# Optimization experiments

Hardware: AMD Instinct MI355X
Metric: run time of the kernel (lower is better)

## Reference

```python
import jax, jax.numpy as jnp
import numpy as np

B = 16384   # batched decode steps (have_action_batch across transitions)
H = 1024    # hidden_dim
A = 20      # len(ner_map) + 2 valid-action vocabulary


def setup_inputs() -> dict:
    key = jax.random.key(0)
    ks = jax.random.split(key, 10)
    scale = 0.02
    buffer_h = jax.random.normal(ks[0], (B, H), jnp.float32)
    stack_h = jax.random.normal(ks[1], (B, H), jnp.float32)
    output_h = jax.random.normal(ks[2], (B, H), jnp.float32)
    action_h = jax.random.normal(ks[3], (B, H), jnp.float32)
    W1 = jax.random.normal(ks[4], (4 * H, H), jnp.float32) * scale  # lstms_output_2_softmax
    b1 = jnp.zeros((H,), jnp.float32)
    W2 = jax.random.normal(ks[5], (H, A), jnp.float32) * scale      # output_2_act
    b2 = jnp.zeros((A,), jnp.float32)
    real_actions = jax.random.randint(ks[6], (B,), 0, A, dtype=jnp.int32)
    valid_mask = jax.random.bernoulli(ks[7], 0.5, (B, A))
    # gold action must always be in the valid-action list
    valid_mask = valid_mask.at[jnp.arange(B), real_actions].set(True)
    return {
        "buffer_h": buffer_h, "stack_h": stack_h, "output_h": output_h,
        "action_h": action_h, "W1": W1, "b1": b1, "W2": W2, "b2": b2,
        "valid_mask": valid_mask, "real_actions": real_actions,
    }


def reference(buffer_h, stack_h, output_h, action_h, W1, b1, W2, b2, valid_mask, real_actions):
    # ragged concat of per-example LSTM states -> [B, 4H]
    x = jnp.concatenate([buffer_h, stack_h, output_h, action_h], axis=1)
    hidden = jnp.tanh(x @ W1 + b1)          # lstms_output_2_softmax + tanh, [B, H]
    logits = hidden @ W2 + b2               # output_2_act, [B, A]
    # per-example valid-action gather expressed as masked log_softmax
    NEG = jnp.asarray(-1e9, logits.dtype)
    masked = jnp.where(valid_mask, logits, NEG)
    log_probs = jax.nn.log_softmax(masked, axis=-1)
    predict_actions = jnp.argmax(log_probs, axis=-1)               # [B] int
    losses = jnp.take_along_axis(log_probs, real_actions[:, None].astype(jnp.int32), axis=1)[:, 0]
    return predict_actions, losses
```

## Files before the change

### kernel.cpp

```cpp
#include <hip/hip_runtime.h>
#include <math.h>


#define BTOT 16384
#define HD   1024
#define NACT 20
#define KTOT 4096
#define KT_N 128

typedef __attribute__((ext_vector_type(8))) short short8;
typedef __attribute__((ext_vector_type(4))) float f32x4;

#define MFMA(a, b, c) __builtin_amdgcn_mfma_f32_16x16x32_bf16((a), (b), (c), 0, 0, 0)

__device__ __forceinline__ void gload16(const void* g, void* l)
{
    auto gp = (const __attribute__((address_space(1))) unsigned int*)((uintptr_t)g);
    auto lp = (__attribute__((address_space(3))) unsigned int*)((uintptr_t)l);
    __builtin_amdgcn_global_load_lds(gp, lp, 16, 0, 0);
}

__device__ __forceinline__ void split8(const float4 v0, const float4 v1,
                                       int4& hi, int4& lo)
{
    const float f[8] = {v0.x, v0.y, v0.z, v0.w, v1.x, v1.y, v1.z, v1.w};
    unsigned hp[4], lp[4];
#pragma unroll
    for (int i = 0; i < 4; ++i) {
        const unsigned u0 = __float_as_uint(f[2 * i]);
        const unsigned u1 = __float_as_uint(f[2 * i + 1]);
        const unsigned r0 = u0 + 0x7FFFu + ((u0 >> 16) & 1u);
        const unsigned r1 = u1 + 0x7FFFu + ((u1 >> 16) & 1u);
        hp[i] = (r0 >> 16) | (r1 & 0xFFFF0000u);
        const float h0 = __uint_as_float(r0 & 0xFFFF0000u);
        const float h1 = __uint_as_float(r1 & 0xFFFF0000u);
        const float d0 = f[2 * i] - h0;
        const float d1 = f[2 * i + 1] - h1;
        const unsigned s0 = __float_as_uint(d0);
        const unsigned s1 = __float_as_uint(d1);
        const unsigned q0 = s0 + 0x7FFFu + ((s0 >> 16) & 1u);
        const unsigned q1 = s1 + 0x7FFFu + ((s1 >> 16) & 1u);
        lp[i] = (q0 >> 16) | (q1 & 0xFFFF0000u);
    }
    hi = make_int4((int)hp[0], (int)hp[1], (int)hp[2], (int)hp[3]);
    lo = make_int4((int)lp[0], (int)lp[1], (int)lp[2], (int)lp[3]);
}

__global__ __launch_bounds__(256) void detect_mask_kernel(
    const unsigned int* __restrict__ w, int nwords, int* __restrict__ ctr)
{
    int c0 = 0, c1 = 0, c2 = 0, c3 = 0;
    for (int i = blockIdx.x * 256 + threadIdx.x; i < nwords; i += gridDim.x * 256) {
        unsigned int v = w[i];
        c0 += (v & 0x000000FFu) ? 1 : 0;
        c1 += (v & 0x0000FF00u) ? 1 : 0;
        c2 += (v & 0x00FF0000u) ? 1 : 0;
        c3 += (v & 0xFF000000u) ? 1 : 0;
    }
#pragma unroll
    for (int off = 32; off; off >>= 1) {
        c0 += __shfl_xor(c0, off, 64);
        c1 += __shfl_xor(c1, off, 64);
        c2 += __shfl_xor(c2, off, 64);
        c3 += __shfl_xor(c3, off, 64);
    }
    if ((threadIdx.x & 63) == 0) {
        atomicAdd(&ctr[0], c0);
        atomicAdd(&ctr[1], c1);
        atomicAdd(&ctr[2], c2);
        atomicAdd(&ctr[3], c3);
    }
}

__global__ __launch_bounds__(256) void wpack_kernel(
    const float* __restrict__ W1, char* __restrict__ Wp)
{
    const int b  = blockIdx.x;
    const int t  = threadIdx.x;
    const int nt = b >> 7;
    const int kt = b & 127;
    const int nn = t & 127;
    const int h  = t >> 7;

    float f[16];
#pragma unroll
    for (int kk = 0; kk < 16; ++kk)
        f[kk] = W1[(size_t)(kt * 32 + h * 16 + kk) * HD + nt * 128 + nn];

    int4 hi0, lo0, hi1, lo1;
    split8(make_float4(f[0], f[1], f[2], f[3]),
           make_float4(f[4], f[5], f[6], f[7]), hi0, lo0);
    split8(make_float4(f[8], f[9], f[10], f[11]),
           make_float4(f[12], f[13], f[14], f[15]), hi1, lo1);

    char* rowp = Wp + (((size_t)(nt * KT_N + kt)) << 14) + nn * 128;
    const int r7 = nn & 7;
    const int s0 = ((2 * h) ^ r7) << 4;
    const int s1 = ((2 * h + 1) ^ r7) << 4;
    *(int4*)(rowp + s0)        = hi0;
    *(int4*)(rowp + s1)        = hi1;
    *(int4*)(rowp + (s0 ^ 64)) = lo0;
    *(int4*)(rowp + (s1 ^ 64)) = lo1;
}


#define PHASE(AP)                                                                   \
    {                                                                               \
        const short8 ah0 = *(const short8*)(bufc + (aBase + (2*(AP)) * 2048));      \
        const short8 al0 = *(const short8*)(bufc + ((aBase + (2*(AP)) * 2048) ^ 64)); \
        const short8 ah1 = *(const short8*)(bufc + (aBase + (2*(AP)+1) * 2048));    \
        const short8 al1 = *(const short8*)(bufc + ((aBase + (2*(AP)+1) * 2048) ^ 64)); \
        __builtin_amdgcn_s_setprio(1);                                              \
        _Pragma("unroll")                                                           \
        for (int nf = 0; nf < 4; ++nf) {                                            \
            acc[2*(AP)][nf]   = MFMA(ah0, bh[nf], acc[2*(AP)][nf]);                 \
            acc[2*(AP)][nf]   = MFMA(ah0, bl[nf], acc[2*(AP)][nf]);                 \
            acc[2*(AP)][nf]   = MFMA(al0, bh[nf], acc[2*(AP)][nf]);                 \
            acc[2*(AP)+1][nf] = MFMA(ah1, bh[nf], acc[2*(AP)+1][nf]);               \
            acc[2*(AP)+1][nf] = MFMA(ah1, bl[nf], acc[2*(AP)+1][nf]);               \
            acc[2*(AP)+1][nf] = MFMA(al1, bh[nf], acc[2*(AP)+1][nf]);               \
        }                                                                           \
        __builtin_amdgcn_s_setprio(0);                                              \
    }

__global__ __launch_bounds__(512, 1) void gemm1_mfma_kernel(
    const float* __restrict__ A0, const float* __restrict__ A1,
    const float* __restrict__ A2, const float* __restrict__ A3,
    const char* __restrict__ Wp, const float* __restrict__ b1,
    float* __restrict__ hidden)
{
    extern __shared__ __align__(16) char smem[];

    const int newbid = (blockIdx.x & 7) * 32 + (blockIdx.x >> 3);
    const int mt = newbid >> 2;
    const int nt = newbid & 3;

    const int t    = threadIdx.x;
    const int lane = t & 63;
    const int wid  = t >> 6;
    const int wr = wid >> 2, wc = wid & 3;
    const int lrow = lane & 15;
    const int lk   = lane >> 4;

    const int stag = (wid ^ (wid >> 2)) & 1;

    const int rowL  = t >> 1;
    const int khalf = t & 1;
    const size_t aRowOff = (size_t)(mt * 256 + rowL) * HD;

    const char* gB0 = Wp + (((size_t)((nt * 2)     * KT_N)) << 14);
    const char* gB1 = Wp + (((size_t)((nt * 2 + 1) * KT_N)) << 14);

    const unsigned aBase = (unsigned)(wr * 128 + lrow) * 128
                         + (((unsigned)lk ^ (unsigned)(lrow & 7)) << 4);
    const unsigned bBase = (unsigned)(wc >> 1) * 16384
                         + (unsigned)((wc & 1) * 64 + lrow) * 128
                         + (((unsigned)lk ^ (unsigned)(lrow & 7)) << 4);

    const int r7 = rowL & 7;
    const unsigned wA0 = (unsigned)rowL * 128 + (((unsigned)(2 * khalf)     ^ (unsigned)r7) << 4);
    const unsigned wA1 = (unsigned)rowL * 128 + (((unsigned)(2 * khalf + 1) ^ (unsigned)r7) << 4);

    f32x4 acc[8][4];
#pragma unroll
    for (int i = 0; i < 8; ++i)
#pragma unroll
        for (int j = 0; j < 4; ++j) acc[i][j] = (f32x4){0.f, 0.f, 0.f, 0.f};

    {
        const float4* ap = (const float4*)(A0 + aRowOff + khalf * 16);
        const float4 f0 = ap[0], f1 = ap[1], f2 = ap[2], f3 = ap[3];
        int4 h0, l0, h1, l1;
        split8(f0, f1, h0, l0);
        split8(f2, f3, h1, l1);
        char* lA = smem;
        *(int4*)(lA + wA0)        = h0;
        *(int4*)(lA + (wA0 ^ 64)) = l0;
        *(int4*)(lA + wA1)        = h1;
        *(int4*)(lA + (wA1 ^ 64)) = l1;
        char* lB = smem + 32768;
        gload16(gB0 + t * 16,        lB + t * 16);
        gload16(gB0 + 8192 + t * 16, lB + 8192 + t * 16);
        gload16(gB1 + t * 16,        lB + 16384 + t * 16);
        gload16(gB1 + 8192 + t * 16, lB + 24576 + t * 16);
    }
    __syncthreads();

    for (int kt = 0; kt < KT_N; ++kt) {
        const int cur = kt & 1;
        const char* bufc  = smem + cur * 65536;
        const char* bufcB = bufc + 32768;
        char*       bufn  = smem + (cur ^ 1) * 65536;
        const bool pref = (kt + 1 < KT_N);

        float4 f0, f1, f2, f3;
        if (pref) {
            char* lB = bufn + 32768;
            const char* s0 = gB0 + (((size_t)(kt + 1)) << 14);
            const char* s1 = gB1 + (((size_t)(kt + 1)) << 14);
            gload16(s0 + t * 16,        lB + t * 16);
            gload16(s0 + 8192 + t * 16, lB + 8192 + t * 16);
            gload16(s1 + t * 16,        lB + 16384 + t * 16);
            gload16(s1 + 8192 + t * 16, lB + 24576 + t * 16);
            const int kg = (kt + 1) * 32 + khalf * 16;
            const float* seg = (kg < 1024) ? A0 : (kg < 2048) ? A1 : (kg < 3072) ? A2 : A3;
            const float4* ap = (const float4*)(seg + aRowOff + (kg & 1023));
            f0 = ap[0]; f1 = ap[1]; f2 = ap[2]; f3 = ap[3];
        }

        short8 bh[4], bl[4];
#pragma unroll
        for (int nf = 0; nf < 4; ++nf) {
            bh[nf] = *(const short8*)(bufcB + (bBase + nf * 2048));
            bl[nf] = *(const short8*)(bufcB + ((bBase + nf * 2048) ^ 64));
        }

        if (stag == 0) {
            PHASE(0) PHASE(1) PHASE(2) PHASE(3)
        } else {
            PHASE(2) PHASE(3) PHASE(0) PHASE(1)
        }

        if (pref) {
            int4 h0, l0, h1, l1;
            split8(f0, f1, h0, l0);
            split8(f2, f3, h1, l1);
            char* wAp = bufn;
            *(int4*)(wAp + wA0)        = h0;
            *(int4*)(wAp + (wA0 ^ 64)) = l0;
            *(int4*)(wAp + wA1)        = h1;
            *(int4*)(wAp + (wA1 ^ 64)) = l1;
        }
        __syncthreads();
    }

#pragma unroll
    for (int nf = 0; nf < 4; ++nf) {
        const int col = nt * 256 + wc * 64 + nf * 16 + lrow;
        const float bias = b1[col];
#pragma unroll
        for (int mf = 0; mf < 8; ++mf) {
            const int row0 = mt * 256 + wr * 128 + mf * 16 + lk * 4;
#pragma unroll
            for (int r = 0; r < 4; ++r)
                hidden[(size_t)(row0 + r) * HD + col] = tanhf(acc[mf][nf][r] + bias);
        }
    }
}

__device__ __forceinline__ void finish_row(
    const float* __restrict__ acc, const float* __restrict__ b2,
    const void* __restrict__ mask, const int* __restrict__ real_actions,
    int fmt, int row, float* __restrict__ out,
    int* __restrict__ flagCnt, int* __restrict__ flagList, int lane)
{
    float masked[NACT];
#pragma unroll
    for (int a = 0; a < NACT; ++a) {
        const float lg = acc[a] + b2[a];
        bool valid;
        if (fmt == 0)      valid = ((const unsigned char*)mask)[(size_t)row * NACT + a] != 0;
        else if (fmt == 1) valid = ((const int*)mask)[(size_t)row * NACT + a] != 0;
        else               valid = ((const float*)mask)[(size_t)row * NACT + a] != 0.f;
        masked[a] = valid ? lg : -1e9f;
    }
    float m = masked[0], m2 = -3e38f;
    int amax = 0;
#pragma unroll
    for (int a = 1; a < NACT; ++a) {
        const float v = masked[a];
        if (v > m) { m2 = m; m = v; amax = a; }
        else if (v > m2) m2 = v;
    }
    float s = 0.f;
#pragma unroll
    for (int a = 0; a < NACT; ++a) s += expf(masked[a] - m);
    const float lse = m + logf(s);
    const int ga = real_actions[row];
    float gl = masked[0];
#pragma unroll
    for (int a = 1; a < NACT; ++a) gl = (ga == a) ? masked[a] : gl;
    if (lane == 0) {
        out[row] = (float)amax;
        out[BTOT + row] = gl - lse;
        if (flagList != nullptr && (m - m2) < 1e-3f) {
            const int ix = atomicAdd(flagCnt, 1);
            flagList[ix] = row;
        }
    }
}

__global__ __launch_bounds__(256) void head_kernel(
    const float* __restrict__ hidden, const float* __restrict__ W2,
    const float* __restrict__ b2, const void* __restrict__ mask,
    const int* __restrict__ real_actions, int* __restrict__ ctr,
    int* __restrict__ flagList, float* __restrict__ out, int rowBase)
{
    const int lane = threadIdx.x & 63;
    const int lr0  = (blockIdx.x * 4 + (threadIdx.x >> 6)) * 2;

    float a0[NACT], a1[NACT];
#pragma unroll
    for (int a = 0; a < NACT; ++a) { a0[a] = 0.f; a1[a] = 0.f; }

    const float* h0 = hidden + (size_t)lr0 * HD;
    const float* h1 = h0 + HD;
#pragma unroll 4
    for (int j = 0; j < 16; ++j) {
        const int h = lane + 64 * j;
        const float hv0 = h0[h];
        const float hv1 = h1[h];
        const float4* w4 = (const float4*)(W2 + (size_t)h * NACT);
        const float4 w0 = w4[0], w1 = w4[1], w2 = w4[2], w3 = w4[3], w4v = w4[4];
        a0[0]  = fmaf(hv0, w0.x,  a0[0]);  a1[0]  = fmaf(hv1, w0.x,  a1[0]);
        a0[1]  = fmaf(hv0, w0.y,  a0[1]);  a1[1]  = fmaf(hv1, w0.y,  a1[1]);
        a0[2]  = fmaf(hv0, w0.z,  a0[2]);  a1[2]  = fmaf(hv1, w0.z,  a1[2]);
        a0[3]  = fmaf(hv0, w0.w,  a0[3]);  a1[3]  = fmaf(hv1, w0.w,  a1[3]);
        a0[4]  = fmaf(hv0, w1.x,  a0[4]);  a1[4]  = fmaf(hv1, w1.x,  a1[4]);
        a0[5]  = fmaf(hv0, w1.y,  a0[5]);  a1[5]  = fmaf(hv1, w1.y,  a1[5]);
        a0[6]  = fmaf(hv0, w1.z,  a0[6]);  a1[6]  = fmaf(hv1, w1.z,  a1[6]);
        a0[7]  = fmaf(hv0, w1.w,  a0[7]);  a1[7]  = fmaf(hv1, w1.w,  a1[7]);
        a0[8]  = fmaf(hv0, w2.x,  a0[8]);  a1[8]  = fmaf(hv1, w2.x,  a1[8]);
        a0[9]  = fmaf(hv0, w2.y,  a0[9]);  a1[9]  = fmaf(hv1, w2.y,  a1[9]);
        a0[10] = fmaf(hv0, w2.z,  a0[10]); a1[10] = fmaf(hv1, w2.z,  a1[10]);
        a0[11] = fmaf(hv0, w2.w,  a0[11]); a1[11] = fmaf(hv1, w2.w,  a1[11]);
        a0[12] = fmaf(hv0, w3.x,  a0[12]); a1[12] = fmaf(hv1, w3.x,  a1[12]);
        a0[13] = fmaf(hv0, w3.y,  a0[13]); a1[13] = fmaf(hv1, w3.y,  a1[13]);
        a0[14] = fmaf(hv0, w3.z,  a0[14]); a1[14] = fmaf(hv1, w3.z,  a1[14]);
        a0[15] = fmaf(hv0, w3.w,  a0[15]); a1[15] = fmaf(hv1, w3.w,  a1[15]);
        a0[16] = fmaf(hv0, w4v.x, a0[16]); a1[16] = fmaf(hv1, w4v.x, a1[16]);
        a0[17] = fmaf(hv0, w4v.y, a0[17]); a1[17] = fmaf(hv1, w4v.y, a1[17]);
        a0[18] = fmaf(hv0, w4v.z, a0[18]); a1[18] = fmaf(hv1, w4v.z, a1[18]);
        a0[19] = fmaf(hv0, w4v.w, a0[19]); a1[19] = fmaf(hv1, w4v.w, a1[19]);
    }
#pragma unroll
    for (int off = 32; off; off >>= 1) {
#pragma unroll
        for (int a = 0; a < NACT; ++a) {
            a0[a] += __shfl_xor(a0[a], off, 64);
            a1[a] += __shfl_xor(a1[a], off, 64);
        }
    }

    const int c1 = ctr[1], c2 = ctr[2], c3 = ctr[3];
    const int fmt = (c1 > 0) ? 0 : ((c2 > 0 || c3 > 0) ? 2 : 1);

    finish_row(a0, b2, mask, real_actions, fmt, rowBase + lr0,     out, &ctr[4], flagList, lane);
    finish_row(a1, b2, mask, real_actions, fmt, rowBase + lr0 + 1, out, &ctr[4], flagList, lane);
}

__global__ __launch_bounds__(256) void refine_hidden_kernel(
    const float* __restrict__ A0, const float* __restrict__ A1,
    const float* __restrict__ A2, const float* __restrict__ A3,
    const float* __restrict__ W1, const float* __restrict__ b1,
    const int* __restrict__ ctr, const int* __restrict__ list,
    float* __restrict__ hiddenR, int cap)
{
    __shared__ float xs[2][KTOT];
    __shared__ float red[2][4][64];
    const int tid = threadIdx.x;
    int count = ctr[4]; if (count > cap) count = cap;
    const int total = ((count + 1) >> 1) << 4;

    for (int u = blockIdx.x; u < total; u += gridDim.x) {
        const int p  = u >> 4;
        const int f0 = 2 * p;
        const int f1 = (2 * p + 1 < count) ? (2 * p + 1) : f0;
        const int r0 = list[f0];
        const int r1 = list[f1];
        const int colBase = (u & 15) << 6;

        for (int i = tid; i < KTOT; i += 256) {
            const float* seg = (i < 1024) ? A0 : (i < 2048) ? A1 : (i < 3072) ? A2 : A3;
            xs[0][i] = seg[(size_t)r0 * HD + (i & 1023)];
            xs[1][i] = seg[(size_t)r1 * HD + (i & 1023)];
        }
        __syncthreads();

        const int col   = colBase + (tid & 63);
        const int kbase = (tid >> 6) << 10;
        const float* Wc = W1 + col;
        float acc0 = 0.f, acc1 = 0.f;

        float wa[16], wb[16];
#pragma unroll
        for (int v = 0; v < 16; ++v) wa[v] = Wc[(size_t)(kbase + v) * HD];
#pragma unroll
        for (int v = 0; v < 16; ++v) wb[v] = Wc[(size_t)(kbase + 16 + v) * HD];

        const int kend = kbase + 1024;
        for (int k0 = kbase; k0 < kend; k0 += 32) {
#pragma unroll
            for (int v = 0; v < 16; ++v) {
                acc0 = fmaf(xs[0][k0 + v], wa[v], acc0);
                acc1 = fmaf(xs[1][k0 + v], wa[v], acc1);
            }
            if (k0 + 32 < kend) {
#pragma unroll
                for (int v = 0; v < 16; ++v)
                    wa[v] = Wc[(size_t)(k0 + 32 + v) * HD];
            }
#pragma unroll
            for (int v = 0; v < 16; ++v) {
                acc0 = fmaf(xs[0][k0 + 16 + v], wb[v], acc0);
                acc1 = fmaf(xs[1][k0 + 16 + v], wb[v], acc1);
            }
            if (k0 + 48 < kend) {
#pragma unroll
                for (int v = 0; v < 16; ++v)
                    wb[v] = Wc[(size_t)(k0 + 48 + v) * HD];
            }
        }

        red[0][tid >> 6][tid & 63] = acc0;
        red[1][tid >> 6][tid & 63] = acc1;
        __syncthreads();

        if (tid < 128) {
            const int r = tid >> 6, c = tid & 63;
            const float s = red[r][0][c] + red[r][1][c] + red[r][2][c] + red[r][3][c];
            const int f = r ? f1 : f0;
            hiddenR[(size_t)f * HD + colBase + c] = tanhf(s + b1[colBase + c]);
        }
        __syncthreads();
    }
}

__global__ __launch_bounds__(256) void refine_head_kernel(
    const float* __restrict__ hiddenR, const float* __restrict__ W2,
    const float* __restrict__ b2, const void* __restrict__ mask,
    const int* __restrict__ real_actions, const int* __restrict__ ctr,
    const int* __restrict__ list, float* __restrict__ out, int cap)
{
    const int lane = threadIdx.x & 63;
    const int wv   = threadIdx.x >> 6;
    int count = ctr[4]; if (count > cap) count = cap;
    const int c1 = ctr[1], c2 = ctr[2], c3 = ctr[3];
    const int fmt = (c1 > 0) ? 0 : ((c2 > 0 || c3 > 0) ? 2 : 1);

    for (int f = blockIdx.x * 4 + wv; f < count; f += gridDim.x * 4) {
        const int row = list[f];
        const float* hrow = hiddenR + (size_t)f * HD;
        float a20[NACT];
#pragma unroll
        for (int a = 0; a < NACT; ++a) a20[a] = 0.f;
#pragma unroll 4
        for (int m = 0; m < 16; ++m) {
            const int h = lane + 64 * m;
            const float hv = hrow[h];
            const float4* w4 = (const float4*)(W2 + (size_t)h * NACT);
            const float4 w0 = w4[0], w1 = w4[1], w2 = w4[2], w3 = w4[3], w4v = w4[4];
            a20[0]  = fmaf(hv, w0.x,  a20[0]);  a20[1]  = fmaf(hv, w0.y,  a20[1]);
            a20[2]  = fmaf(hv, w0.z,  a20[2]);  a20[3]  = fmaf(hv, w0.w,  a20[3]);
            a20[4]  = fmaf(hv, w1.x,  a20[4]);  a20[5]  = fmaf(hv, w1.y,  a20[5]);
            a20[6]  = fmaf(hv, w1.z,  a20[6]);  a20[7]  = fmaf(hv, w1.w,  a20[7]);
            a20[8]  = fmaf(hv, w2.x,  a20[8]);  a20[9]  = fmaf(hv, w2.y,  a20[9]);
            a20[10] = fmaf(hv, w2.z,  a20[10]); a20[11] = fmaf(hv, w2.w,  a20[11]);
            a20[12] = fmaf(hv, w3.x,  a20[12]); a20[13] = fmaf(hv, w3.y,  a20[13]);
            a20[14] = fmaf(hv, w3.z,  a20[14]); a20[15] = fmaf(hv, w3.w,  a20[15]);
            a20[16] = fmaf(hv, w4v.x, a20[16]); a20[17] = fmaf(hv, w4v.y, a20[17]);
            a20[18] = fmaf(hv, w4v.z, a20[18]); a20[19] = fmaf(hv, w4v.w, a20[19]);
        }
#pragma unroll
        for (int off = 32; off; off >>= 1) {
#pragma unroll
            for (int a = 0; a < NACT; ++a) a20[a] += __shfl_xor(a20[a], off, 64);
        }
        finish_row(a20, b2, mask, real_actions, fmt, row, out, nullptr, nullptr, lane);
    }
}

extern "C" void kernel_launch(void* const* d_in, const int* in_sizes, int n_in,
                              void* d_out, int out_size, void* d_ws, size_t ws_size,
                              hipStream_t stream)
{
    const float* buf_h = (const float*)d_in[0];
    const float* stk_h = (const float*)d_in[1];
    const float* out_h = (const float*)d_in[2];
    const float* act_h = (const float*)d_in[3];
    const float* W1    = (const float*)d_in[4];
    const float* b1    = (const float*)d_in[5];
    const float* W2    = (const float*)d_in[6];
    const float* b2    = (const float*)d_in[7];
    const void*  mask  = d_in[8];
    const int*   ra    = (const int*)d_in[9];
    float*       out   = (float*)d_out;

    int*  ctr      = (int*)d_ws;
    int*  flagList = (int*)((char*)d_ws + 256);
    char* Wp       = (char*)d_ws + 256 + 65536;
    const size_t wpBytes = (size_t)8 * KT_N * 16384;
    float* hidden  = (float*)(Wp + wpBytes);

    hipMemsetAsync(d_ws, 0, 256, stream);
    detect_mask_kernel<<<64, 256, 0, stream>>>(
        (const unsigned int*)mask, BTOT * NACT / 4, ctr);
    wpack_kernel<<<8 * KT_N, 256, 0, stream>>>(W1, Wp);

    hipFuncSetAttribute((const void*)gemm1_mfma_kernel,
                        hipFuncAttributeMaxDynamicSharedMemorySize, 131072);

    gemm1_mfma_kernel<<<256, 512, 131072, stream>>>(
        buf_h, stk_h, out_h, act_h, Wp, b1, hidden);
    head_kernel<<<BTOT / 8, 256, 0, stream>>>(
        hidden, W2, b2, mask, ra, ctr, flagList, out, 0);

    float* hiddenR = hidden;
    refine_hidden_kernel<<<2048, 256, 0, stream>>>(
        buf_h, stk_h, out_h, act_h, W1, b1, ctr, flagList, hiddenR, BTOT);
    refine_head_kernel<<<64, 256, 0, stream>>>(
        hiddenR, W2, b2, mask, ra, ctr, flagList, out, BTOT);
}
```

Measured before the change: 528.5 us.

## Prefetch A tile two steps ahead and remap blocks to XCDs by column tile

The GEMM1 main loop now loads the fp32 A tile two k-steps ahead into rotating registers and splits and writes it to LDS before the MFMA phase, not after. This gives global load latency a full iteration to resolve and takes the split/LDS store off the tail behind the MFMAs. The block-to-tile mapping also changes so each XCD handles a single N tile and half of the M tiles, which changes L2 sharing of W and A. The cost is extra registers for the second A buffer under a 512-thread, one-block launch bound, which may cause spills.

```diff
diff --git a/kernel.cpp b/kernel.cpp
--- a/kernel.cpp
+++ b/kernel.cpp
@@ -123,6 +123,46 @@
         __builtin_amdgcn_s_setprio(0);                                              \
     }
 
+#define STEP(KT, CUR, NXT)                                                          \
+    {                                                                               \
+        const int curb = (KT) & 1;                                                  \
+        const char* bufc  = smem + curb * 65536;                                    \
+        const char* bufcB = bufc + 32768;                                           \
+        char*       bufn  = smem + (curb ^ 1) * 65536;                              \
+        if ((KT) + 2 < KT_N) {                                                      \
+            const int kg = ((KT) + 2) * 32 + khalf * 16;                            \
+            const float* seg = (kg < 1024) ? A0 : (kg < 2048) ? A1                  \
+                               : (kg < 3072) ? A2 : A3;                             \
+            const float4* ap = (const float4*)(seg + aRowOff + (kg & 1023));        \
+            NXT[0] = ap[0]; NXT[1] = ap[1]; NXT[2] = ap[2]; NXT[3] = ap[3];         \
+        }                                                                           \
+        if ((KT) + 1 < KT_N) {                                                      \
+            char* lB = bufn + 32768;                                                \
+            const char* s0 = gB0 + (((size_t)((KT) + 1)) << 14);                    \
+            const char* s1 = gB1 + (((size_t)((KT) + 1)) << 14);                    \
+            gload16(s0 + t * 16,        lB + t * 16);                               \
+            gload16(s0 + 8192 + t * 16, lB + 8192 + t * 16);                        \
+            gload16(s1 + t * 16,        lB + 16384 + t * 16);                       \
+            gload16(s1 + 8192 + t * 16, lB + 24576 + t * 16);                       \
+            int4 h0, l0, h1, l1;                                                    \
+            split8(CUR[0], CUR[1], h0, l0);                                         \
+            split8(CUR[2], CUR[3], h1, l1);                                         \
+            *(int4*)(bufn + wA0)        = h0;                                       \
+            *(int4*)(bufn + (wA0 ^ 64)) = l0;                                       \
+            *(int4*)(bufn + wA1)        = h1;                                       \
+            *(int4*)(bufn + (wA1 ^ 64)) = l1;                                       \
+        }                                                                           \
+        short8 bh[4], bl[4];                                                        \
+        _Pragma("unroll")                                                           \
+        for (int nf = 0; nf < 4; ++nf) {                                            \
+            bh[nf] = *(const short8*)(bufcB + (bBase + nf * 2048));                 \
+            bl[nf] = *(const short8*)(bufcB + ((bBase + nf * 2048) ^ 64));          \
+        }                                                                           \
+        if (stag == 0) { PHASE(0) PHASE(1) PHASE(2) PHASE(3) }                      \
+        else           { PHASE(2) PHASE(3) PHASE(0) PHASE(1) }                      \
+        __syncthreads();                                                            \
+    }
+
 __global__ __launch_bounds__(512, 1) void gemm1_mfma_kernel(
     const float* __restrict__ A0, const float* __restrict__ A1,
     const float* __restrict__ A2, const float* __restrict__ A3,
@@ -131,9 +171,9 @@
 {
     extern __shared__ __align__(16) char smem[];
 
-    const int newbid = (blockIdx.x & 7) * 32 + (blockIdx.x >> 3);
-    const int mt = newbid >> 2;
-    const int nt = newbid & 3;
+    const int xcd = blockIdx.x & 7;
+    const int nt  = xcd & 3;
+    const int mt  = (blockIdx.x >> 3) + ((xcd >> 2) << 5);
 
     const int t    = threadIdx.x;
     const int lane = t & 63;
@@ -167,17 +207,20 @@
 #pragma unroll
         for (int j = 0; j < 4; ++j) acc[i][j] = (f32x4){0.f, 0.f, 0.f, 0.f};
 
+    float4 rA0[4], rA1[4];
+
     {
         const float4* ap = (const float4*)(A0 + aRowOff + khalf * 16);
         const float4 f0 = ap[0], f1 = ap[1], f2 = ap[2], f3 = ap[3];
         int4 h0, l0, h1, l1;
         split8(f0, f1, h0, l0);
         split8(f2, f3, h1, l1);
-        char* lA = smem;
-        *(int4*)(lA + wA0)        = h0;
-        *(int4*)(lA + (wA0 ^ 64)) = l0;
-        *(int4*)(lA + wA1)        = h1;
-        *(int4*)(lA + (wA1 ^ 64)) = l1;
+        *(int4*)(smem + wA0)        = h0;
+        *(int4*)(smem + (wA0 ^ 64)) = l0;
+        *(int4*)(smem + wA1)        = h1;
+        *(int4*)(smem + (wA1 ^ 64)) = l1;
+        const float4* ap1 = (const float4*)(A0 + aRowOff + 32 + khalf * 16);
+        rA0[0] = ap1[0]; rA0[1] = ap1[1]; rA0[2] = ap1[2]; rA0[3] = ap1[3];
         char* lB = smem + 32768;
         gload16(gB0 + t * 16,        lB + t * 16);
         gload16(gB0 + 8192 + t * 16, lB + 8192 + t * 16);
@@ -186,52 +229,9 @@
     }
     __syncthreads();
 
-    for (int kt = 0; kt < KT_N; ++kt) {
-        const int cur = kt & 1;
-        const char* bufc  = smem + cur * 65536;
-        const char* bufcB = bufc + 32768;
-        char*       bufn  = smem + (cur ^ 1) * 65536;
-        const bool pref = (kt + 1 < KT_N);
-
-        float4 f0, f1, f2, f3;
-        if (pref) {
-            char* lB = bufn + 32768;
-            const char* s0 = gB0 + (((size_t)(kt + 1)) << 14);
-            const char* s1 = gB1 + (((size_t)(kt + 1)) << 14);
-            gload16(s0 + t * 16,        lB + t * 16);
-            gload16(s0 + 8192 + t * 16, lB + 8192 + t * 16);
-            gload16(s1 + t * 16,        lB + 16384 + t * 16);
-            gload16(s1 + 8192 + t * 16, lB + 24576 + t * 16);
-            const int kg = (kt + 1) * 32 + khalf * 16;
-            const float* seg = (kg < 1024) ? A0 : (kg < 2048) ? A1 : (kg < 3072) ? A2 : A3;
-            const float4* ap = (const float4*)(seg + aRowOff + (kg & 1023));
-            f0 = ap[0]; f1 = ap[1]; f2 = ap[2]; f3 = ap[3];
-        }
-
-        short8 bh[4], bl[4];
-#pragma unroll
-        for (int nf = 0; nf < 4; ++nf) {
-            bh[nf] = *(const short8*)(bufcB + (bBase + nf * 2048));
-            bl[nf] = *(const short8*)(bufcB + ((bBase + nf * 2048) ^ 64));
-        }
-
-        if (stag == 0) {
-            PHASE(0) PHASE(1) PHASE(2) PHASE(3)
-        } else {
-            PHASE(2) PHASE(3) PHASE(0) PHASE(1)
-        }
-
-        if (pref) {
-            int4 h0, l0, h1, l1;
-            split8(f0, f1, h0, l0);
-            split8(f2, f3, h1, l1);
-            char* wAp = bufn;
-            *(int4*)(wAp + wA0)        = h0;
-            *(int4*)(wAp + (wA0 ^ 64)) = l0;
-            *(int4*)(wAp + wA1)        = h1;
-            *(int4*)(wAp + (wA1 ^ 64)) = l1;
-        }
-        __syncthreads();
+    for (int kt2 = 0; kt2 < KT_N; kt2 += 2) {
+        STEP(kt2,     rA0, rA1)
+        STEP(kt2 + 1, rA1, rA0)
     }
 
 #pragma unroll
```

Result: slower. 1.921 ms (+263.5%).
